# Kernel optimization log

Hardware: AMD Instinct MI355X
Metric: run time of the kernel (lower is better)

The kernel has to match this reference:

```python
import jax, jax.numpy as jnp
import numpy as np

SMOOTHNESS_RATIO = 0.2
DEGREE_RATIO = 0.1
SPARSITY_RATIO = 0.1
VERY_SMALL_NUMBER = 1e-12


def setup_inputs() -> dict:
    key = jax.random.key(0)
    k1, k2 = jax.random.split(key)
    B, N, D = 64, 1024, 16
    out_adj = jax.random.uniform(k1, (B, N, N), dtype=jnp.float32)  # nonneg adjacency (softmax-like)
    features = jax.random.normal(k2, (B, N, D), dtype=jnp.float32)
    return {"out_adj": out_adj, "features": features}


def reference(out_adj, features):
    # Faithful fused version of add_batch_graph_loss with keep_batch_dim=True.
    # Per sample i: smoothness_ratio * tr(F^T (diag(deg) - A) F) / (N*N)
    #   tr(F^T diag(deg) F) = sum_n deg_n ||f_n||^2
    #   tr(F^T A F)        = sum(F * (A @ F))
    B, N, _ = out_adj.shape
    denom = jnp.float32(N * N)

    deg = jnp.sum(out_adj, axis=-1)                       # [B, N] row degrees
    AF = jnp.einsum('bij,bjd->bid', out_adj, features)    # [B, N, D]
    smooth = (jnp.einsum('bn,bnd->b', deg, features * features)
              - jnp.einsum('bnd,bnd->b', features, AF))   # [B] = tr(F^T L F)
    graph_loss = SMOOTHNESS_RATIO * smooth / denom

    # degree regularization: -degree_ratio * ones^T log(A @ ones + eps) / N
    # A @ ones == deg
    log_degrees = jnp.log(deg + VERY_SMALL_NUMBER)        # [B, N]
    graph_loss = graph_loss - DEGREE_RATIO * jnp.sum(log_degrees, axis=-1) / N

    # sparsity: sparsity_ratio * sum(A^2) / (N*N)
    graph_loss = graph_loss + SPARSITY_RATIO * jnp.sum(out_adj * out_adj, axis=(1, 2)) / denom
    return graph_loss  # [B]
```

## Files before the change

kernel.cpp:

```cpp
#include <hip/hip_runtime.h>


#define NN      1024
#define DD      16
#define ROWS    64
#define TPB     256
#define SMOOTHR 0.2f
#define DEGRR   0.1f
#define SPARSR  0.1f
#define EPSV    1e-12f

typedef float vf4 __attribute__((ext_vector_type(4)));

__global__ __launch_bounds__(TPB)
void graph_loss_kernel(const float* __restrict__ A,
                       const float* __restrict__ F,
                       float* __restrict__ out) {
    __shared__ float fn2_lds[ROWS];
    __shared__ float degq[ROWS][65];
    __shared__ float wred[4][2];

    const int tid = threadIdx.x;
    const int bid = blockIdx.x;
    const int b   = bid >> 4;
    const int n0  = (bid & 15) * ROWS;

    const float* __restrict__ Fb = F + (size_t)b * NN * DD;
    const float* __restrict__ Ab = A + ((size_t)b * NN + n0) * NN;

    vf4 fj[4][4];
    {
        const float* p = Fb + (size_t)(4 * tid) * DD;
        #pragma unroll
        for (int jj = 0; jj < 4; ++jj)
            #pragma unroll
            for (int q = 0; q < 4; ++q)
                fj[jj][q] = *(const vf4*)(p + jj * DD + 4 * q);
    }

    if (tid < ROWS) {
        const float* p = Fb + (size_t)(n0 + tid) * DD;
        float s = 0.f;
        #pragma unroll
        for (int d = 0; d < DD; ++d) s += p[d] * p[d];
        fn2_lds[tid] = s;
    }
    __syncthreads();

    float sm = 0.f, sq = 0.f;

    const float* __restrict__ arow = Ab + 4 * tid;
    const int  g       = tid >> 2;
    const bool deglane = (tid & 3) == 0;

    #define LOADR(r) __builtin_nontemporal_load((const vf4*)(arow + (size_t)(r) * NN))
    vf4 a0 = LOADR(0);
    vf4 a1 = LOADR(1);

    #pragma unroll 1
    for (int r = 0; r < ROWS; ++r) {
        const vf4 a = a0;
        a0 = a1;
        if (r + 2 < ROWS) a1 = LOADR(r + 2);

        const vf4* __restrict__ Fr = (const vf4*)(Fb + (size_t)(n0 + r) * DD);
        const vf4 f0 = Fr[0], f1 = Fr[1], f2 = Fr[2], f3 = Fr[3];
        const float fn2 = fn2_lds[r];

        float s = (a.x + a.y) + (a.z + a.w);
        s += __shfl_xor(s, 1);
        s += __shfl_xor(s, 2);
        if (deglane) degq[r][g] = s;

        sq += a.x * a.x + a.y * a.y + a.z * a.z + a.w * a.w;

        float dt0, dt1, dt2, dt3;
        dt0  = fj[0][0].x * f0.x + fj[0][0].y * f0.y + fj[0][0].z * f0.z + fj[0][0].w * f0.w;
        dt0 += fj[0][1].x * f1.x + fj[0][1].y * f1.y + fj[0][1].z * f1.z + fj[0][1].w * f1.w;
        dt0 += fj[0][2].x * f2.x + fj[0][2].y * f2.y + fj[0][2].z * f2.z + fj[0][2].w * f2.w;
        dt0 += fj[0][3].x * f3.x + fj[0][3].y * f3.y + fj[0][3].z * f3.z + fj[0][3].w * f3.w;
        dt1  = fj[1][0].x * f0.x + fj[1][0].y * f0.y + fj[1][0].z * f0.z + fj[1][0].w * f0.w;
        dt1 += fj[1][1].x * f1.x + fj[1][1].y * f1.y + fj[1][1].z * f1.z + fj[1][1].w * f1.w;
        dt1 += fj[1][2].x * f2.x + fj[1][2].y * f2.y + fj[1][2].z * f2.z + fj[1][2].w * f2.w;
        dt1 += fj[1][3].x * f3.x + fj[1][3].y * f3.y + fj[1][3].z * f3.z + fj[1][3].w * f3.w;
        dt2  = fj[2][0].x * f0.x + fj[2][0].y * f0.y + fj[2][0].z * f0.z + fj[2][0].w * f0.w;
        dt2 += fj[2][1].x * f1.x + fj[2][1].y * f1.y + fj[2][1].z * f1.z + fj[2][1].w * f1.w;
        dt2 += fj[2][2].x * f2.x + fj[2][2].y * f2.y + fj[2][2].z * f2.z + fj[2][2].w * f2.w;
        dt2 += fj[2][3].x * f3.x + fj[2][3].y * f3.y + fj[2][3].z * f3.z + fj[2][3].w * f3.w;
        dt3  = fj[3][0].x * f0.x + fj[3][0].y * f0.y + fj[3][0].z * f0.z + fj[3][0].w * f0.w;
        dt3 += fj[3][1].x * f1.x + fj[3][1].y * f1.y + fj[3][1].z * f1.z + fj[3][1].w * f1.w;
        dt3 += fj[3][2].x * f2.x + fj[3][2].y * f2.y + fj[3][2].z * f2.z + fj[3][2].w * f2.w;
        dt3 += fj[3][3].x * f3.x + fj[3][3].y * f3.y + fj[3][3].z * f3.z + fj[3][3].w * f3.w;

        sm += a.x * (fn2 - dt0) + a.y * (fn2 - dt1)
            + a.z * (fn2 - dt2) + a.w * (fn2 - dt3);
    }
    #undef LOADR

    __syncthreads();
    float lg = 0.f;
    if (tid < ROWS) {
        float s = 0.f;
        #pragma unroll 1
        for (int i = 0; i < ROWS; ++i) s += degq[tid][i];
        lg = logf(s + EPSV);
    }

    #pragma unroll
    for (int m = 1; m < 64; m <<= 1) {
        sm += __shfl_xor(sm, m);
        sq += __shfl_xor(sq, m);
        lg += __shfl_xor(lg, m);
    }
    const int w = tid >> 6;
    if ((tid & 63) == 0) { wred[w][0] = sm; wred[w][1] = sq; }
    __syncthreads();
    if (tid == 0) {
        float S = 0.f, Q = 0.f;
        #pragma unroll
        for (int i = 0; i < 4; ++i) { S += wred[i][0]; Q += wred[i][1]; }
        const float denom = (float)NN * (float)NN;
        const float contrib = SMOOTHR * S / denom
                            - DEGRR * lg / (float)NN
                            + SPARSR * Q / denom;
        atomicAdd(out + b, contrib);
    }
}

extern "C" void kernel_launch(void* const* d_in, const int* in_sizes, int n_in,
                              void* d_out, int out_size, void* d_ws, size_t ws_size,
                              hipStream_t stream) {
    const float* A = (const float*)d_in[0];
    const float* F = (const float*)d_in[1];
    float* out = (float*)d_out;

    const int B = out_size;
    (void)hipMemsetAsync(d_out, 0, (size_t)B * sizeof(float), stream);
    graph_loss_kernel<<<dim3(B * (NN / ROWS)), dim3(TPB), 0, stream>>>(A, F, out);
}
```

Before: 367.0 us.

## Accumulate A^T·F_rows per column then dot with F, staging row features in LDS

The per-row 16-wide dot products between column and row features are replaced by accumulating a 4x16 weighted feature sum per thread across rows, followed by one final dot with the column features. The degree term is computed from row degrees times squared row norms. Row features are staged in LDS, A loads are prefetched four rows deep, and launch bounds now request 4 blocks per SM. This lowers FMA work per A element, which suits a memory-bound kernel, but float summation order changes.

Result: slower. 754.3 us (+105.5%).

```diff
diff --git a/kernel.cpp b/kernel.cpp
--- a/kernel.cpp
+++ b/kernel.cpp
@@ -12,11 +12,11 @@
 
 typedef float vf4 __attribute__((ext_vector_type(4)));
 
-__global__ __launch_bounds__(TPB)
+__global__ __launch_bounds__(TPB, 4)
 void graph_loss_kernel(const float* __restrict__ A,
                        const float* __restrict__ F,
                        float* __restrict__ out) {
-    __shared__ float fn2_lds[ROWS];
+    __shared__ float fLDS[ROWS][DD];
     __shared__ float degq[ROWS][65];
     __shared__ float wred[4][2];
 
@@ -28,99 +28,122 @@
     const float* __restrict__ Fb = F + (size_t)b * NN * DD;
     const float* __restrict__ Ab = A + ((size_t)b * NN + n0) * NN;
 
-    vf4 fj[4][4];
+    ((vf4*)fLDS)[tid] = *(const vf4*)(Fb + (size_t)n0 * DD + 4 * tid);
+    __syncthreads();
+
+    vf4 w[4][4];
+    #pragma unroll
+    for (int jj = 0; jj < 4; ++jj)
+        #pragma unroll
+        for (int q = 0; q < 4; ++q)
+            w[jj][q] = (vf4){0.f, 0.f, 0.f, 0.f};
+
+    float sq = 0.f;
+    const float* __restrict__ arow = Ab + 4 * tid;
+    const int  g       = tid >> 2;
+    const bool deglane = (tid & 3) == 0;
+
+    #define LOADR(r) __builtin_nontemporal_load((const vf4*)(arow + (size_t)(r) * NN))
+    #define LDF(dst, rr)                                                     \
+        do {                                                                 \
+            dst##0 = *(const vf4*)&fLDS[(rr)][0];                            \
+            dst##1 = *(const vf4*)&fLDS[(rr)][4];                            \
+            dst##2 = *(const vf4*)&fLDS[(rr)][8];                            \
+            dst##3 = *(const vf4*)&fLDS[(rr)][12];                           \
+        } while (0)
+    #define COMPUTE(av, f0v, f1v, f2v, f3v, rr)                              \
+        do {                                                                 \
+            float s_ = (av.x + av.y) + (av.z + av.w);                        \
+            s_ += __shfl_xor(s_, 1);                                         \
+            s_ += __shfl_xor(s_, 2);                                         \
+            if (deglane) degq[(rr)][g] = s_;                                 \
+            sq += av.x * av.x + av.y * av.y + av.z * av.z + av.w * av.w;     \
+            w[0][0] += av.x * f0v; w[1][0] += av.y * f0v;                    \
+            w[2][0] += av.z * f0v; w[3][0] += av.w * f0v;                    \
+            w[0][1] += av.x * f1v; w[1][1] += av.y * f1v;                    \
+            w[2][1] += av.z * f1v; w[3][1] += av.w * f1v;                    \
+            w[0][2] += av.x * f2v; w[1][2] += av.y * f2v;                    \
+            w[2][2] += av.z * f2v; w[3][2] += av.w * f2v;                    \
+            w[0][3] += av.x * f3v; w[1][3] += av.y * f3v;                    \
+            w[2][3] += av.z * f3v; w[3][3] += av.w * f3v;                    \
+        } while (0)
+
+    vf4 a0 = LOADR(0);
+    vf4 a1 = LOADR(1);
+    vf4 a2 = LOADR(2);
+    vf4 a3 = LOADR(3);
+    vf4 fA0, fA1, fA2, fA3, fB0, fB1, fB2, fB3;
+    LDF(fA, 0);
+
+    #pragma unroll 1
+    for (int r = 0; r < ROWS - 4; r += 4) {
+        LDF(fB, r + 1);
+        COMPUTE(a0, fA0, fA1, fA2, fA3, r);
+        a0 = LOADR(r + 4);
+        LDF(fA, r + 2);
+        COMPUTE(a1, fB0, fB1, fB2, fB3, r + 1);
+        a1 = LOADR(r + 5);
+        LDF(fB, r + 3);
+        COMPUTE(a2, fA0, fA1, fA2, fA3, r + 2);
+        a2 = LOADR(r + 6);
+        LDF(fA, r + 4);
+        COMPUTE(a3, fB0, fB1, fB2, fB3, r + 3);
+        a3 = LOADR(r + 7);
+    }
+    LDF(fB, ROWS - 3);
+    COMPUTE(a0, fA0, fA1, fA2, fA3, ROWS - 4);
+    LDF(fA, ROWS - 2);
+    COMPUTE(a1, fB0, fB1, fB2, fB3, ROWS - 3);
+    LDF(fB, ROWS - 1);
+    COMPUTE(a2, fA0, fA1, fA2, fA3, ROWS - 2);
+    COMPUTE(a3, fB0, fB1, fB2, fB3, ROWS - 1);
+
+    #undef LOADR
+    #undef LDF
+    #undef COMPUTE
+
+    __syncthreads();
+    float lg = 0.f, dfn = 0.f;
+    if (tid < ROWS) {
+        float s = 0.f;
+        #pragma unroll 1
+        for (int i = 0; i < ROWS; ++i) s += degq[tid][i];
+        lg = logf(s + EPSV);
+        float t = 0.f;
+        #pragma unroll
+        for (int d = 0; d < DD; ++d) { const float v = fLDS[tid][d]; t += v * v; }
+        dfn = s * t;
+    }
+
+    float dot = 0.f;
     {
         const float* p = Fb + (size_t)(4 * tid) * DD;
         #pragma unroll
         for (int jj = 0; jj < 4; ++jj)
             #pragma unroll
-            for (int q = 0; q < 4; ++q)
-                fj[jj][q] = *(const vf4*)(p + jj * DD + 4 * q);
-    }
-
-    if (tid < ROWS) {
-        const float* p = Fb + (size_t)(n0 + tid) * DD;
-        float s = 0.f;
-        #pragma unroll
-        for (int d = 0; d < DD; ++d) s += p[d] * p[d];
-        fn2_lds[tid] = s;
-    }
-    __syncthreads();
-
-    float sm = 0.f, sq = 0.f;
-
-    const float* __restrict__ arow = Ab + 4 * tid;
-    const int  g       = tid >> 2;
-    const bool deglane = (tid & 3) == 0;
-
-    #define LOADR(r) __builtin_nontemporal_load((const vf4*)(arow + (size_t)(r) * NN))
-    vf4 a0 = LOADR(0);
-    vf4 a1 = LOADR(1);
-
-    #pragma unroll 1
-    for (int r = 0; r < ROWS; ++r) {
-        const vf4 a = a0;
-        a0 = a1;
-        if (r + 2 < ROWS) a1 = LOADR(r + 2);
-
-        const vf4* __restrict__ Fr = (const vf4*)(Fb + (size_t)(n0 + r) * DD);
-        const vf4 f0 = Fr[0], f1 = Fr[1], f2 = Fr[2], f3 = Fr[3];
-        const float fn2 = fn2_lds[r];
-
-        float s = (a.x + a.y) + (a.z + a.w);
-        s += __shfl_xor(s, 1);
-        s += __shfl_xor(s, 2);
-        if (deglane) degq[r][g] = s;
-
-        sq += a.x * a.x + a.y * a.y + a.z * a.z + a.w * a.w;
-
-        float dt0, dt1, dt2, dt3;
-        dt0  = fj[0][0].x * f0.x + fj[0][0].y * f0.y + fj[0][0].z * f0.z + fj[0][0].w * f0.w;
-        dt0 += fj[0][1].x * f1.x + fj[0][1].y * f1.y + fj[0][1].z * f1.z + fj[0][1].w * f1.w;
-        dt0 += fj[0][2].x * f2.x + fj[0][2].y * f2.y + fj[0][2].z * f2.z + fj[0][2].w * f2.w;
-        dt0 += fj[0][3].x * f3.x + fj[0][3].y * f3.y + fj[0][3].z * f3.z + fj[0][3].w * f3.w;
-        dt1  = fj[1][0].x * f0.x + fj[1][0].y * f0.y + fj[1][0].z * f0.z + fj[1][0].w * f0.w;
-        dt1 += fj[1][1].x * f1.x + fj[1][1].y * f1.y + fj[1][1].z * f1.z + fj[1][1].w * f1.w;
-        dt1 += fj[1][2].x * f2.x + fj[1][2].y * f2.y + fj[1][2].z * f2.z + fj[1][2].w * f2.w;
-        dt1 += fj[1][3].x * f3.x + fj[1][3].y * f3.y + fj[1][3].z * f3.z + fj[1][3].w * f3.w;
-        dt2  = fj[2][0].x * f0.x + fj[2][0].y * f0.y + fj[2][0].z * f0.z + fj[2][0].w * f0.w;
-        dt2 += fj[2][1].x * f1.x + fj[2][1].y * f1.y + fj[2][1].z * f1.z + fj[2][1].w * f1.w;
-        dt2 += fj[2][2].x * f2.x + fj[2][2].y * f2.y + fj[2][2].z * f2.z + fj[2][2].w * f2.w;
-        dt2 += fj[2][3].x * f3.x + fj[2][3].y * f3.y + fj[2][3].z * f3.z + fj[2][3].w * f3.w;
-        dt3  = fj[3][0].x * f0.x + fj[3][0].y * f0.y + fj[3][0].z * f0.z + fj[3][0].w * f0.w;
-        dt3 += fj[3][1].x * f1.x + fj[3][1].y * f1.y + fj[3][1].z * f1.z + fj[3][1].w * f1.w;
-        dt3 += fj[3][2].x * f2.x + fj[3][2].y * f2.y + fj[3][2].z * f2.z + fj[3][2].w * f2.w;
-        dt3 += fj[3][3].x * f3.x + fj[3][3].y * f3.y + fj[3][3].z * f3.z + fj[3][3].w * f3.w;
-
-        sm += a.x * (fn2 - dt0) + a.y * (fn2 - dt1)
-            + a.z * (fn2 - dt2) + a.w * (fn2 - dt3);
-    }
-    #undef LOADR
-
-    __syncthreads();
-    float lg = 0.f;
-    if (tid < ROWS) {
-        float s = 0.f;
-        #pragma unroll 1
-        for (int i = 0; i < ROWS; ++i) s += degq[tid][i];
-        lg = logf(s + EPSV);
+            for (int q = 0; q < 4; ++q) {
+                const vf4 f = *(const vf4*)(p + jj * DD + 4 * q);
+                dot += f.x * w[jj][q].x + f.y * w[jj][q].y
+                     + f.z * w[jj][q].z + f.w * w[jj][q].w;
+            }
     }
 
     #pragma unroll
     for (int m = 1; m < 64; m <<= 1) {
-        sm += __shfl_xor(sm, m);
-        sq += __shfl_xor(sq, m);
-        lg += __shfl_xor(lg, m);
+        dot += __shfl_xor(dot, m);
+        sq  += __shfl_xor(sq, m);
+        lg  += __shfl_xor(lg, m);
+        dfn += __shfl_xor(dfn, m);
     }
-    const int w = tid >> 6;
-    if ((tid & 63) == 0) { wred[w][0] = sm; wred[w][1] = sq; }
+    const int wv = tid >> 6;
+    if ((tid & 63) == 0) { wred[wv][0] = dot; wred[wv][1] = sq; }
     __syncthreads();
     if (tid == 0) {
-        float S = 0.f, Q = 0.f;
+        float Dt = 0.f, Q = 0.f;
         #pragma unroll
-        for (int i = 0; i < 4; ++i) { S += wred[i][0]; Q += wred[i][1]; }
+        for (int i = 0; i < 4; ++i) { Dt += wred[i][0]; Q += wred[i][1]; }
         const float denom = (float)NN * (float)NN;
-        const float contrib = SMOOTHR * S / denom
+        const float contrib = SMOOTHR * (dfn - Dt) / denom
                             - DEGRR * lg / (float)NN
                             + SPARSR * Q / denom;
         atomicAdd(out + b, contrib);
```
